# Performance work log

Measured on AMD Instinct MI355X. Metric: run time of the kernel, lower is better.

Reference implementation:

```python
import jax, jax.numpy as jnp
import numpy as np

S = 4      # num_residual_streams
I = 1      # num_branch_inputs
DIM = 2048
LAYER_INDEX = 0


def setup_inputs() -> dict:
    key = jax.random.key(0)
    ks = jax.random.split(key, 6)
    residuals = jax.random.normal(ks[0], (16, 2048, DIM), dtype=jnp.float32)
    # RMSNorm weight (init 1.0, small noise for non-trivial math)
    norm_weight = 1.0 + 0.02 * jax.random.normal(ks[1], (DIM,), dtype=jnp.float32)
    # static_beta: ones[S, I]
    static_beta = jnp.ones((S, I), dtype=jnp.float32) + 0.02 * jax.random.normal(ks[2], (S, I), dtype=jnp.float32)
    # static_alpha: cat([alpha0 (one-hot row at layer_index), eye(S)], dim=1) -> [S, I+S]
    alpha0 = jnp.zeros((S, I), dtype=jnp.float32).at[LAYER_INDEX, :].set(1.0)
    static_alpha = jnp.concatenate([alpha0, jnp.eye(S, dtype=jnp.float32)], axis=1)
    dynamic_alpha_fn = 0.02 * jax.random.normal(ks[3], (DIM, S + I), dtype=jnp.float32)
    dynamic_alpha_scale = jnp.float32(0.01)
    dynamic_beta_fn = 0.02 * jax.random.normal(ks[4], (DIM, I), dtype=jnp.float32)
    dynamic_beta_scale = jnp.float32(0.01)
    return dict(residuals=residuals, norm_weight=norm_weight, static_alpha=static_alpha,
                static_beta=static_beta, dynamic_alpha_fn=dynamic_alpha_fn,
                dynamic_alpha_scale=dynamic_alpha_scale, dynamic_beta_fn=dynamic_beta_fn,
                dynamic_beta_scale=dynamic_beta_scale)


def reference(residuals, norm_weight, static_alpha, static_beta,
              dynamic_alpha_fn, dynamic_alpha_scale, dynamic_beta_fn, dynamic_beta_scale):
    bs, L, D = residuals.shape
    b = bs // S
    # '(b s) l d -> b l s d'  (stream index is the inner factor of the leading axis)
    x = residuals.reshape(b, S, L, D).transpose(0, 2, 1, 3)  # [b, L, S, D]

    # RMSNorm over last dim (torch default eps = finfo.eps)
    eps = jnp.finfo(x.dtype).eps
    normed = x * jax.lax.rsqrt(jnp.mean(x * x, axis=-1, keepdims=True) + eps) * norm_weight

    # width connection
    alpha = jnp.tanh(normed @ dynamic_alpha_fn) * dynamic_alpha_scale + static_alpha  # [b,L,S,S+I]
    beta = jnp.tanh(normed @ dynamic_beta_fn) * dynamic_beta_scale + static_beta      # [b,L,S,I]
    mix_h = jnp.einsum('blst,blsd->bltd', alpha, x)                                   # [b,L,S+I,D]

    branch_input = mix_h[..., :I, :]   # [b,L,I,D]
    res = mix_h[..., I:, :]            # [b,L,S,D]

    # branch is identity; 'b l i d -> i b l d'
    branch_out = branch_input.transpose(2, 0, 1, 3)  # [I,b,L,D]

    # depth connection
    res = jnp.einsum('ibld,blsi->blsd', branch_out, beta) + res  # [b,L,S,D]
    # 'b l s d -> (b s) l d'
    out = res.transpose(0, 2, 1, 3).reshape(b * S, L, D)
    return out
```

## Files before the change

### kernel.cpp

```cpp
#include <hip/hip_runtime.h>


#define DD 2048
#define NS 4
#define NT 5
#define NW 8
#define ROWSTRIDE ((size_t)DD * 2048)

typedef float v4f __attribute__((ext_vector_type(4)));

__global__ void prep_kernel(const float* __restrict__ w,
                            const float* __restrict__ A,
                            const float* __restrict__ Bfn,
                            float* __restrict__ WA,
                            float* __restrict__ WB) {
    int d = blockIdx.x * blockDim.x + threadIdx.x;
    if (d >= DD) return;
    float wf = w[d];
#pragma unroll
    for (int t = 0; t < NT; ++t)
        WA[t * DD + d] = wf * A[d * NT + t];
    WB[d] = wf * Bfn[d];
}

__device__ __forceinline__ float dot4(v4f a, v4f b) {
    return fmaf(a.x, b.x, fmaf(a.y, b.y, fmaf(a.z, b.z, a.w * b.w)));
}

__global__ __launch_bounds__(512, 6) void hyper_kernel(
    const float* __restrict__ X,
    const float* __restrict__ WA,
    const float* __restrict__ WB,
    const float* __restrict__ sA,
    const float* __restrict__ sB,
    const float* __restrict__ aS,
    const float* __restrict__ bS,
    float* __restrict__ out)
{
    __shared__ float shP[NW][NS][7];

    const int g  = blockIdx.x;
    const int bb = g >> 11;
    const int l  = g & 2047;
    const int wv = threadIdx.x >> 6;
    const int ln = threadIdx.x & 63;
    const int d0 = (wv << 8) + (ln << 2);

    const size_t base = ((size_t)(bb * NS) * 2048 + (size_t)l) * (size_t)DD + (size_t)d0;

    v4f xv[NS];
#pragma unroll
    for (int s = 0; s < NS; ++s)
        xv[s] = *(const v4f*)(X + base + (size_t)s * ROWSTRIDE);

    v4f wt[6];
#pragma unroll
    for (int t = 0; t < NT; ++t)
        wt[t] = *(const v4f*)(WA + t * DD + d0);
    wt[5] = *(const v4f*)(WB + d0);

    float acc[NS][7];
#pragma unroll
    for (int s = 0; s < NS; ++s) {
#pragma unroll
        for (int t = 0; t < 6; ++t)
            acc[s][t] = dot4(xv[s], wt[t]);
        acc[s][6] = dot4(xv[s], xv[s]);
    }

#pragma unroll
    for (int m = 1; m < 64; m <<= 1) {
#pragma unroll
        for (int s = 0; s < NS; ++s)
#pragma unroll
            for (int k = 0; k < 7; ++k)
                acc[s][k] += __shfl_xor(acc[s][k], m);
    }

    if (ln == 0) {
#pragma unroll
        for (int s = 0; s < NS; ++s)
#pragma unroll
            for (int k = 0; k < 7; ++k)
                shP[wv][s][k] = acc[s][k];
    }
    __syncthreads();

    const float ascale = aS[0];
    const float bscale = bS[0];
    float val = 0.f;
    if (ln < 24) {
        const bool isA = ln < 20;
        const int s   = isA ? (ln / 5) : (ln - 20);
        const int idx = isA ? (ln % 5) : 5;
        float dv = 0.f, sv = 0.f;
#pragma unroll
        for (int w = 0; w < NW; ++w) {
            dv += shP[w][s][idx];
            sv += shP[w][s][6];
        }
        const float rms = rsqrtf(sv * (1.0f / 2048.0f) + 1.1920929e-07f);
        const float th  = tanhf(rms * dv);
        val = isA ? fmaf(th, ascale, sA[ln]) : fmaf(th, bscale, sB[s]);
    }

    float bet[NS];
#pragma unroll
    for (int s = 0; s < NS; ++s) bet[s] = __shfl(val, 20 + s);

    float c[NS][NS];
#pragma unroll
    for (int sp = 0; sp < NS; ++sp) {
        const float a0 = __shfl(val, sp * 5);
#pragma unroll
        for (int s = 0; s < NS; ++s)
            c[s][sp] = fmaf(bet[s], a0, __shfl(val, sp * 5 + s + 1));
    }

#pragma unroll
    for (int s = 0; s < NS; ++s) {
        v4f o = c[s][0] * xv[0] + c[s][1] * xv[1] + c[s][2] * xv[2] + c[s][3] * xv[3];
        __builtin_nontemporal_store(o, (v4f*)(out + base + (size_t)s * ROWSTRIDE));
    }
}

extern "C" void kernel_launch(void* const* d_in, const int* in_sizes, int n_in,
                              void* d_out, int out_size, void* d_ws, size_t ws_size,
                              hipStream_t stream) {
    const float* X   = (const float*)d_in[0];
    const float* w   = (const float*)d_in[1];
    const float* sA  = (const float*)d_in[2];
    const float* sB  = (const float*)d_in[3];
    const float* Afn = (const float*)d_in[4];
    const float* aSc = (const float*)d_in[5];
    const float* Bfn = (const float*)d_in[6];
    const float* bSc = (const float*)d_in[7];
    float* out = (float*)d_out;

    float* WA = (float*)d_ws;
    float* WB = WA + 5 * 2048;

    prep_kernel<<<8, 256, 0, stream>>>(w, Afn, Bfn, WA, WB);
    hyper_kernel<<<4 * 2048, 512, 0, stream>>>(X, WA, WB, sA, sB, aSc, bSc, out);
}
```

Baseline: 489.8 us.

## Replace per-wave shuffle reductions with LDS transpose and split cross-wave reduction

Every wave used to butterfly-reduce all 28 partial sums with shuffles (28 values times 6 steps). Now each wave writes its partials to LDS as seven float4 chunks. Seven waves then each sum one chunk across all eight waves and do a single float4 shuffle reduction, which cuts shuffle instructions roughly sevenfold. The cost is about 57KB of LDS per block, which lowers achievable occupancy, and the launch-bounds hint drops from 6 to 4 to match. The output stores also switch from nontemporal to regular stores.

```diff
diff --git a/kernel.cpp b/kernel.cpp
--- a/kernel.cpp
+++ b/kernel.cpp
@@ -27,7 +27,7 @@
     return fmaf(a.x, b.x, fmaf(a.y, b.y, fmaf(a.z, b.z, a.w * b.w)));
 }
 
-__global__ __launch_bounds__(512, 6) void hyper_kernel(
+__global__ __launch_bounds__(512, 4) void hyper_kernel(
     const float* __restrict__ X,
     const float* __restrict__ WA,
     const float* __restrict__ WB,
@@ -37,7 +37,8 @@
     const float* __restrict__ bS,
     float* __restrict__ out)
 {
-    __shared__ float shP[NW][NS][7];
+    __shared__ __align__(16) v4f  part[7][NW][64];
+    __shared__ __align__(16) float shS[28];
 
     const int g  = blockIdx.x;
     const int bb = g >> 11;
@@ -59,30 +60,38 @@
         wt[t] = *(const v4f*)(WA + t * DD + d0);
     wt[5] = *(const v4f*)(WB + d0);
 
-    float acc[NS][7];
+    float acc[28];
 #pragma unroll
     for (int s = 0; s < NS; ++s) {
 #pragma unroll
         for (int t = 0; t < 6; ++t)
-            acc[s][t] = dot4(xv[s], wt[t]);
-        acc[s][6] = dot4(xv[s], xv[s]);
+            acc[s * 7 + t] = dot4(xv[s], wt[t]);
+        acc[s * 7 + 6] = dot4(xv[s], xv[s]);
     }
 
 #pragma unroll
-    for (int m = 1; m < 64; m <<= 1) {
+    for (int c = 0; c < 7; ++c) {
+        v4f p;
+        p.x = acc[4 * c + 0]; p.y = acc[4 * c + 1];
+        p.z = acc[4 * c + 2]; p.w = acc[4 * c + 3];
+        part[c][wv][ln] = p;
+    }
+    __syncthreads();
+
+    if (wv < 7) {
+        v4f t4 = part[wv][0][ln];
 #pragma unroll
-        for (int s = 0; s < NS; ++s)
+        for (int j = 1; j < NW; ++j)
+            t4 += part[wv][j][ln];
 #pragma unroll
-            for (int k = 0; k < 7; ++k)
-                acc[s][k] += __shfl_xor(acc[s][k], m);
-    }
-
-    if (ln == 0) {
-#pragma unroll
-        for (int s = 0; s < NS; ++s)
-#pragma unroll
-            for (int k = 0; k < 7; ++k)
-                shP[wv][s][k] = acc[s][k];
+        for (int m = 1; m < 64; m <<= 1) {
+            t4.x += __shfl_xor(t4.x, m);
+            t4.y += __shfl_xor(t4.y, m);
+            t4.z += __shfl_xor(t4.z, m);
+            t4.w += __shfl_xor(t4.w, m);
+        }
+        if (ln == 0)
+            *(v4f*)&shS[4 * wv] = t4;
     }
     __syncthreads();
 
@@ -93,12 +102,8 @@
         const bool isA = ln < 20;
         const int s   = isA ? (ln / 5) : (ln - 20);
         const int idx = isA ? (ln % 5) : 5;
-        float dv = 0.f, sv = 0.f;
-#pragma unroll
-        for (int w = 0; w < NW; ++w) {
-            dv += shP[w][s][idx];
-            sv += shP[w][s][6];
-        }
+        const float dv = shS[s * 7 + idx];
+        const float sv = shS[s * 7 + 6];
         const float rms = rsqrtf(sv * (1.0f / 2048.0f) + 1.1920929e-07f);
         const float th  = tanhf(rms * dv);
         val = isA ? fmaf(th, ascale, sA[ln]) : fmaf(th, bscale, sB[s]);
@@ -120,7 +125,7 @@
 #pragma unroll
     for (int s = 0; s < NS; ++s) {
         v4f o = c[s][0] * xv[0] + c[s][1] * xv[1] + c[s][2] * xv[2] + c[s][3] * xv[3];
-        __builtin_nontemporal_store(o, (v4f*)(out + base + (size_t)s * ROWSTRIDE));
+        *(v4f*)(out + base + (size_t)s * ROWSTRIDE) = o;
     }
 }
 
```

After: 460.7 us. 5.9% less time.
